# Kernel optimization log

Hardware: AMD Instinct MI355X
Metric: run time of the kernel (lower is better)

The kernel has to match this reference:

```python
import jax, jax.numpy as jnp
import numpy as np

N = 1024
H = 128


def setup_inputs() -> dict:
    key = jax.random.key(0)
    k1, k2, k3, k4, k5, k6 = jax.random.split(key, 6)
    s = 1.0 / np.sqrt(H)
    return {
        "node_feats": jax.random.normal(k1, (N, H), dtype=jnp.float32),
        "edge_attr": jax.random.normal(k2, (N * N, H), dtype=jnp.float32),
        "We": jax.random.uniform(k3, (H, H), jnp.float32, -s, s),
        "be": jax.random.uniform(k4, (H,), jnp.float32, -s, s),
        "Wi": jax.random.uniform(k5, (H, H), jnp.float32, -s, s),
        "Wj": jax.random.uniform(k6, (H, H), jnp.float32, -s, s),
    }


def reference(node_feats, edge_attr, We, be, Wi, Wj):
    # f_ij: [N^2, H] linear with bias
    f_ij = edge_attr @ We.T + be
    # f_i, f_j: [N, H] linears without bias
    f_i = node_feats @ Wi.T
    f_j = node_feats @ Wj.T
    # torch.matmul on 1-D vectors -> scalar dot; broadcast into each H-wide row.
    dots = jnp.einsum("ih,jh->ij", f_i, f_j)  # [N, N]
    fi_fj = dots.reshape(-1, 1)                 # [N^2, 1], broadcasts over H
    return jax.nn.relu(f_ij + fi_fj)
```

## Files before the change

### kernel.cpp

```cpp
#include <hip/hip_runtime.h>
#include <hip/hip_bf16.h>
#include <stdint.h>
#include <stddef.h>

typedef __bf16 bf16_t;
typedef __bf16 bf16x8 __attribute__((ext_vector_type(8)));
typedef float  f32x4  __attribute__((ext_vector_type(4)));
typedef float  f32x16 __attribute__((ext_vector_type(16)));

#define NN 1024
#define H  128
#define GRID 2048

__global__ void k_cvt_we(const float* __restrict__ src, bf16_t* __restrict__ dst) {
    int i = blockIdx.x * 256 + threadIdx.x;
    if (i < H * H) dst[i] = (bf16_t)src[i];
}

__global__ void k_proj(const float* __restrict__ node,
                       const float* __restrict__ Wi,
                       const float* __restrict__ Wj,
                       bf16_t* __restrict__ fi,
                       bf16_t* __restrict__ fj) {
    __shared__ float nrow[H];
    const int row = blockIdx.x;
    const int t   = threadIdx.x;
    const int h   = t & (H - 1);
    const int sel = t >> 7;
    if (t < H) nrow[t] = node[(size_t)row * H + t];
    __syncthreads();
    const float* w = (sel ? Wj : Wi) + (size_t)h * H;
    float acc = 0.f;
    #pragma unroll
    for (int k4 = 0; k4 < H / 4; ++k4) {
        f32x4 wv = *(const f32x4*)(w + k4 * 4);
        f32x4 nv = *(const f32x4*)(&nrow[k4 * 4]);
        acc += nv[0] * wv[0] + nv[1] * wv[1] + nv[2] * wv[2] + nv[3] * wv[3];
    }
    bf16_t* dst = sel ? fj : fi;
    dst[(size_t)row * H + h] = (bf16_t)acc;
}

__global__ __launch_bounds__(256, 4)
void k_dots(const bf16_t* __restrict__ fi,
            const bf16_t* __restrict__ fj,
            float* __restrict__ dots) {
    const int t    = threadIdx.x;
    const int wave = t >> 6;
    const int lane = t & 63;
    const int l15  = lane & 15;
    const int g    = lane >> 4;

    const int bm    = blockIdx.x >> 3;
    const int bn    = blockIdx.x & 7;
    const int ibase = bm * 64 + wave * 16;
    const int jbase = bn * 128;

    f32x4 acc[8];
    #pragma unroll
    for (int nt = 0; nt < 8; ++nt) acc[nt] = (f32x4){0.f, 0.f, 0.f, 0.f};

    const bf16_t* a = fi + (size_t)(ibase + l15) * H + g * 8;

    #pragma unroll
    for (int kst = 0; kst < 4; ++kst) {
        bf16x8 af = *(const bf16x8*)(a + kst * 32);
        #pragma unroll
        for (int nt = 0; nt < 8; ++nt) {
            bf16x8 bf = *(const bf16x8*)(fj + (size_t)(jbase + nt * 16 + l15) * H + kst * 32 + g * 8);
            acc[nt] = __builtin_amdgcn_mfma_f32_16x16x32_bf16(af, bf, acc[nt], 0, 0, 0);
        }
    }

    const int rbase = ibase + g * 4;
    #pragma unroll
    for (int r = 0; r < 4; ++r)
        #pragma unroll
        for (int nt = 0; nt < 8; ++nt)
            dots[(size_t)(rbase + r) * NN + jbase + nt * 16 + l15] = acc[nt][r];
}

__device__ __forceinline__ void gl_lds16(const float* g, float* l) {
    __builtin_amdgcn_global_load_lds(
        (const __attribute__((address_space(1))) unsigned int*)g,
        (__attribute__((address_space(3))) unsigned int*)l,
        16, 0, 0);
}

__global__ __launch_bounds__(128, 1)
void k_main(const float* __restrict__ edge,
            const bf16_t* __restrict__ web,
            const float* __restrict__ be,
            const float* __restrict__ dots,
            float* __restrict__ out) {
    __shared__ __align__(16) float ebuf[2][2][32][H];
    __shared__ __align__(16) float dbuf[2][512];

    const int t    = threadIdx.x;
    const int wave = t >> 6;
    const int lane = t & 63;
    const int l31  = lane & 31;
    const int h    = lane >> 5;
    const size_t base = (size_t)blockIdx.x * 512;

    bf16x8 wfr[4][8];
    {
        const bf16_t* wp = web + (size_t)l31 * H + h * 8;
        #pragma unroll
        for (int nt = 0; nt < 4; ++nt)
            #pragma unroll
            for (int kk = 0; kk < 8; ++kk)
                wfr[nt][kk] = *(const bf16x8*)(wp + (size_t)(nt * 32) * H + kk * 16);
    }
    float bias[4];
    #pragma unroll
    for (int nt = 0; nt < 4; ++nt) bias[nt] = be[nt * 32 + l31];

    #pragma unroll
    for (int nt = 0; nt < 4; ++nt) {
        #pragma unroll
        for (int kk = 0; kk < 8; ++kk)
            asm volatile("" : "+v"(wfr[nt][kk]));
        asm volatile("" : "+v"(bias[nt]));
    }

    gl_lds16(dots + base + lane * 4,       &dbuf[wave][0]);
    gl_lds16(dots + base + 256 + lane * 4, &dbuf[wave][256]);

    #define STAGE(K, BI)                                                         \
        {                                                                        \
            const char* tb = (const char*)(edge + (base + (size_t)(K) * 64 + wave * 32) * H); \
            _Pragma("unroll")                                                    \
            for (int i = 0; i < 16; ++i) {                                       \
                const int rr = 2 * i + h;                                        \
                gl_lds16((const float*)(tb + rr * 512 + ((l31 * 16) ^ ((rr & 7) << 4))), \
                         &ebuf[BI][wave][2 * i][0]);                             \
            }                                                                    \
        }

    STAGE(0, 0)

    const int sw = (l31 & 7) << 4;

    #pragma unroll
    for (int k = 0; k < 8; ++k) {
        if (k == 0) asm volatile("s_waitcnt vmcnt(0)"  ::: "memory");
        else        asm volatile("s_waitcnt vmcnt(48)" ::: "memory");
        __builtin_amdgcn_sched_barrier(0);

        const char* erow = (const char*)&ebuf[k & 1][wave][0][0] + l31 * 512;
        f32x4 ua[8], ub[8];
        #pragma unroll
        for (int kk = 0; kk < 8; ++kk) {
            ua[kk] = *(const f32x4*)(erow + ((kk * 64 + h * 32 +  0) ^ sw));
            ub[kk] = *(const f32x4*)(erow + ((kk * 64 + h * 32 + 16) ^ sw));
        }

        if (k < 7) {
            if (k & 1) { STAGE(k + 1, 0) }
            else       { STAGE(k + 1, 1) }
        }

        const float* dl = &dbuf[wave][k * 64 + wave * 32];
        f32x4 dv[4];
        #pragma unroll
        for (int b = 0; b < 4; ++b)
            dv[b] = *(const f32x4*)(dl + 4 * h + 8 * b);

        f32x16 acc[4];
        #pragma unroll
        for (int nt = 0; nt < 4; ++nt)
            #pragma unroll
            for (int r = 0; r < 16; ++r)
                acc[nt][r] = bias[nt] + dv[r >> 2][r & 3];

        #pragma unroll
        for (int kk = 0; kk < 8; ++kk) {
            bf16x8 af;
            #pragma unroll
            for (int e = 0; e < 4; ++e) {
                af[e]     = (bf16_t)ua[kk][e];
                af[e + 4] = (bf16_t)ub[kk][e];
            }
            #pragma unroll
            for (int nt = 0; nt < 4; ++nt)
                acc[nt] = __builtin_amdgcn_mfma_f32_32x32x16_bf16(af, wfr[nt][kk], acc[nt], 0, 0, 0);
        }

        float* orow = out + (base + (size_t)k * 64 + wave * 32 + 4 * h) * H + l31;
        #pragma unroll
        for (int nt = 0; nt < 4; ++nt)
            #pragma unroll
            for (int r = 0; r < 16; ++r)
                orow[((r & 3) + 8 * (r >> 2)) * H + nt * 32] = fmaxf(acc[nt][r], 0.f);
    }
    #undef STAGE
}

extern "C" void kernel_launch(void* const* d_in, const int* in_sizes, int n_in,
                              void* d_out, int out_size, void* d_ws, size_t ws_size,
                              hipStream_t stream) {
    const float* node = (const float*)d_in[0];
    const float* edge = (const float*)d_in[1];
    const float* We   = (const float*)d_in[2];
    const float* be   = (const float*)d_in[3];
    const float* Wi   = (const float*)d_in[4];
    const float* Wj   = (const float*)d_in[5];
    float* out = (float*)d_out;

    char* w = (char*)d_ws;
    bf16_t* fi_bf = (bf16_t*)w;
    bf16_t* fj_bf = (bf16_t*)(w + (256 << 10));
    float*  dots  = (float*)(w + (512 << 10));
    bf16_t* web   = (bf16_t*)(w + (512 << 10) + (4 << 20));

    k_cvt_we<<<(H * H + 255) / 256, 256, 0, stream>>>(We, web);
    k_proj<<<NN, 256, 0, stream>>>(node, Wi, Wj, fi_bf, fj_bf);
    k_dots<<<128, 256, 0, stream>>>(fi_bf, fj_bf, dots);
    k_main<<<GRID, 128, 0, stream>>>(edge, web, be, dots, out);
}
```

Baseline: 242.8 us.

## Split main GEMM across four waves in 2x2 M/N layout with shared tiles

The main kernel now uses 256 threads with four waves arranged 2x2 over rows and output columns, each wave holding half the We fragments. Edge tiles are loaded cooperatively into shared double buffers and synchronised with __syncthreads instead of per-wave vmcnt waits. The aim is to cut register pressure and raise occupancy so more memory traffic is in flight. In exchange it adds block-wide barriers, makes each wave read edge rows that another wave loaded, and drops the manual unroll and scheduling hints.

```diff
diff --git a/kernel.cpp b/kernel.cpp
--- a/kernel.cpp
+++ b/kernel.cpp
@@ -87,89 +87,83 @@
         16, 0, 0);
 }
 
-__global__ __launch_bounds__(128, 1)
+__global__ __launch_bounds__(256)
 void k_main(const float* __restrict__ edge,
             const bf16_t* __restrict__ web,
             const float* __restrict__ be,
             const float* __restrict__ dots,
             float* __restrict__ out) {
-    __shared__ __align__(16) float ebuf[2][2][32][H];
-    __shared__ __align__(16) float dbuf[2][512];
+    __shared__ __align__(16) float bufA[64][H];
+    __shared__ __align__(16) float bufB[64][H];
+    __shared__ float ldots[512];
 
     const int t    = threadIdx.x;
-    const int wave = t >> 6;
+    const int w    = t >> 6;
     const int lane = t & 63;
     const int l31  = lane & 31;
     const int h    = lane >> 5;
+    const int wm   = w & 1;
+    const int wn   = w >> 1;
     const size_t base = (size_t)blockIdx.x * 512;
 
-    bf16x8 wfr[4][8];
+    ldots[t]       = dots[base + t];
+    ldots[256 + t] = dots[base + 256 + t];
+
+    bf16x8 wfr[2][8];
     {
-        const bf16_t* wp = web + (size_t)l31 * H + h * 8;
-        #pragma unroll
-        for (int nt = 0; nt < 4; ++nt)
+        const bf16_t* wp = web + (size_t)(wn * 64 + l31) * H + h * 8;
+        #pragma unroll
+        for (int nt = 0; nt < 2; ++nt)
             #pragma unroll
             for (int kk = 0; kk < 8; ++kk)
                 wfr[nt][kk] = *(const bf16x8*)(wp + (size_t)(nt * 32) * H + kk * 16);
     }
-    float bias[4];
-    #pragma unroll
-    for (int nt = 0; nt < 4; ++nt) bias[nt] = be[nt * 32 + l31];
-
-    #pragma unroll
-    for (int nt = 0; nt < 4; ++nt) {
-        #pragma unroll
-        for (int kk = 0; kk < 8; ++kk)
-            asm volatile("" : "+v"(wfr[nt][kk]));
-        asm volatile("" : "+v"(bias[nt]));
-    }
-
-    gl_lds16(dots + base + lane * 4,       &dbuf[wave][0]);
-    gl_lds16(dots + base + 256 + lane * 4, &dbuf[wave][256]);
-
-    #define STAGE(K, BI)                                                         \
+    float bias[2];
+    #pragma unroll
+    for (int nt = 0; nt < 2; ++nt) bias[nt] = be[wn * 64 + nt * 32 + l31];
+
+    #define STAGE(K, BUFP)                                                       \
         {                                                                        \
-            const char* tb = (const char*)(edge + (base + (size_t)(K) * 64 + wave * 32) * H); \
+            const char* tb = (const char*)(edge + (base + (size_t)(K) * 64) * H); \
             _Pragma("unroll")                                                    \
-            for (int i = 0; i < 16; ++i) {                                       \
-                const int rr = 2 * i + h;                                        \
+            for (int i = 0; i < 8; ++i) {                                        \
+                const int rr = w * 16 + 2 * i + h;                               \
                 gl_lds16((const float*)(tb + rr * 512 + ((l31 * 16) ^ ((rr & 7) << 4))), \
-                         &ebuf[BI][wave][2 * i][0]);                             \
+                         &BUFP[w * 16 + 2 * i][0]);                              \
             }                                                                    \
         }
 
-    STAGE(0, 0)
+    STAGE(0, bufA)
 
     const int sw = (l31 & 7) << 4;
 
-    #pragma unroll
+    #pragma unroll 1
     for (int k = 0; k < 8; ++k) {
-        if (k == 0) asm volatile("s_waitcnt vmcnt(0)"  ::: "memory");
-        else        asm volatile("s_waitcnt vmcnt(48)" ::: "memory");
-        __builtin_amdgcn_sched_barrier(0);
-
-        const char* erow = (const char*)&ebuf[k & 1][wave][0][0] + l31 * 512;
+        __syncthreads();
+
+        const char* crow = (const char*)((k & 1) ? &bufB[0][0] : &bufA[0][0])
+                         + (wm * 32 + l31) * 512;
+
         f32x4 ua[8], ub[8];
         #pragma unroll
         for (int kk = 0; kk < 8; ++kk) {
-            ua[kk] = *(const f32x4*)(erow + ((kk * 64 + h * 32 +  0) ^ sw));
-            ub[kk] = *(const f32x4*)(erow + ((kk * 64 + h * 32 + 16) ^ sw));
+            ua[kk] = *(const f32x4*)(crow + ((kk * 64 + h * 32 +  0) ^ sw));
+            ub[kk] = *(const f32x4*)(crow + ((kk * 64 + h * 32 + 16) ^ sw));
         }
 
         if (k < 7) {
-            if (k & 1) { STAGE(k + 1, 0) }
-            else       { STAGE(k + 1, 1) }
-        }
-
-        const float* dl = &dbuf[wave][k * 64 + wave * 32];
+            if (k & 1) { STAGE(k + 1, bufA) }
+            else       { STAGE(k + 1, bufB) }
+        }
+
         f32x4 dv[4];
         #pragma unroll
         for (int b = 0; b < 4; ++b)
-            dv[b] = *(const f32x4*)(dl + 4 * h + 8 * b);
-
-        f32x16 acc[4];
-        #pragma unroll
-        for (int nt = 0; nt < 4; ++nt)
+            dv[b] = *(const f32x4*)(&ldots[k * 64 + wm * 32 + 4 * h + 8 * b]);
+
+        f32x16 acc[2];
+        #pragma unroll
+        for (int nt = 0; nt < 2; ++nt)
             #pragma unroll
             for (int r = 0; r < 16; ++r)
                 acc[nt][r] = bias[nt] + dv[r >> 2][r & 3];
@@ -183,13 +177,13 @@
                 af[e + 4] = (bf16_t)ub[kk][e];
             }
             #pragma unroll
-            for (int nt = 0; nt < 4; ++nt)
+            for (int nt = 0; nt < 2; ++nt)
                 acc[nt] = __builtin_amdgcn_mfma_f32_32x32x16_bf16(af, wfr[nt][kk], acc[nt], 0, 0, 0);
         }
 
-        float* orow = out + (base + (size_t)k * 64 + wave * 32 + 4 * h) * H + l31;
-        #pragma unroll
-        for (int nt = 0; nt < 4; ++nt)
+        float* orow = out + (base + (size_t)k * 64 + wm * 32 + 4 * h) * H + wn * 64 + l31;
+        #pragma unroll
+        for (int nt = 0; nt < 2; ++nt)
             #pragma unroll
             for (int r = 0; r < 16; ++r)
                 orow[((r & 3) + 8 * (r >> 2)) * H + nt * 32] = fmaxf(acc[nt][r], 0.f);
@@ -217,5 +211,5 @@
     k_cvt_we<<<(H * H + 255) / 256, 256, 0, stream>>>(We, web);
     k_proj<<<NN, 256, 0, stream>>>(node, Wi, Wj, fi_bf, fj_bf);
     k_dots<<<128, 256, 0, stream>>>(fi_bf, fj_bf, dots);
-    k_main<<<GRID, 128, 0, stream>>>(edge, web, be, dots, out);
-}
+    k_main<<<GRID, 256, 0, stream>>>(edge, web, be, dots, out);
+}
```

New measurement: 237.3 us. -2.3%, faster.
